# Performance work log

Hardware: AMD Instinct MI355X
Metric: run time of the kernel (lower is better)

Reference implementation:

```python
import jax, jax.numpy as jnp
import numpy as np

B, T, DA, DZ, K = 2048, 256, 20, 4, 3


def setup_inputs() -> dict:
    key = jax.random.key(0)
    k1, k2, k3, k4 = jax.random.split(key, 4)
    a = jax.random.normal(k1, (B, T, DA), dtype=jnp.float32)
    alpha_logits = jax.random.normal(k2, (B, T, K), dtype=jnp.float32)
    # original inits: A = eye per mixture component, C = 0.05*randn
    A_base = jnp.tile(jnp.eye(DZ, dtype=jnp.float32), (K, 1, 1)) \
             + 0.01 * jax.random.normal(k3, (K, DZ, DZ), dtype=jnp.float32)
    C_base = 0.05 * jax.random.normal(k4, (K, DA, DZ), dtype=jnp.float32)
    return {"a": a, "alpha_logits": alpha_logits, "A_base": A_base, "C_base": C_base}


def _kvae_smooth(a, alpha_logits, A_base, C_base):
    alpha = jax.nn.softmax(alpha_logits, axis=-1)          # [B,T,K]
    Q = 0.08 * jnp.eye(DZ, dtype=a.dtype)
    R = 0.03 * jnp.eye(DA, dtype=a.dtype)
    std_min = 1e-4 * jnp.eye(DZ, dtype=a.dtype)
    I_z = jnp.eye(DZ, dtype=a.dtype)
    z0 = jnp.zeros((B, DZ), dtype=a.dtype)
    std0 = 20.0 * jnp.broadcast_to(I_z, (B, DZ, DZ))

    def filt_step(carry, xs):
        z_prev, std_prev = carry                            # [B,dz], [B,dz,dz]
        a_t, alpha_t = xs                                   # [B,da], [B,K]
        Ai = jnp.einsum('bk,kij->bij', alpha_t, A_base)     # [B,dz,dz]
        Ci = jnp.einsum('bk,kij->bij', alpha_t, C_base)     # [B,da,dz]
        # --- prediction ---
        z_hat = jnp.einsum('bij,bj->bi', Ai, z_prev)
        std_hat = Ai @ std_prev @ Ai.transpose(0, 2, 1) + Q
        std_hat_c = jnp.maximum(std_hat, std_min)           # stored (clipped) version
        # --- update (uses unclipped std_hat, as in the original) ---
        resid = a_t - jnp.einsum('bij,bj->bi', Ci, z_hat)
        S = Ci @ std_hat @ Ci.transpose(0, 2, 1) + R        # [B,da,da]
        Kg = std_hat @ Ci.transpose(0, 2, 1) @ jnp.linalg.inv(S)
        post_z = z_hat + jnp.einsum('bij,bj->bi', Kg, resid)
        IKC = I_z - Kg @ Ci
        post_std = IKC @ std_hat @ IKC.transpose(0, 2, 1) + Kg @ R @ Kg.transpose(0, 2, 1)
        return (post_z, post_std), (z_hat, std_hat_c, post_z, post_std, Ai)

    _, (z_hat_a, std_hat_a, post_z_a, post_std_a, A_a) = jax.lax.scan(
        filt_step, (z0, std0), (a.transpose(1, 0, 2), alpha.transpose(1, 0, 2)))
    # stacked arrays are time-major: [T, B, ...]

    last_z, last_std = post_z_a[-1], post_std_a[-1]

    def smooth_step(carry, xs):
        pz_s, ps_s = carry
        post_z_jm1, post_std_jm1, A_j, std_hat_j, z_hat_j = xs
        D = post_std_jm1 @ A_j.transpose(0, 2, 1) @ jnp.linalg.inv(std_hat_j)
        z_s = post_z_jm1 + jnp.einsum('bij,bj->bi', D, pz_s - z_hat_j)
        s_s = post_std_jm1 + D @ (ps_s - std_hat_j) @ D.transpose(0, 2, 1)
        return (z_s, s_s), (z_s, s_s)

    xs = (post_z_a[:-1], post_std_a[:-1], A_a[1:], std_hat_a[1:], z_hat_a[1:])
    _, (z_sm, s_sm) = jax.lax.scan(smooth_step, (last_z, last_std), xs, reverse=True)
    # z_sm: [T-1, B, dz] in forward time order; append last filtered state
    z_smooth = jnp.concatenate([z_sm, last_z[None]], axis=0).transpose(1, 0, 2)          # [B,T,dz]
    std_smooth = jnp.concatenate([s_sm, last_std[None]], axis=0).transpose(1, 0, 2, 3)   # [B,T,dz,dz]
    return z_smooth, std_smooth


def reference(a, alpha_logits, A_base, C_base):
    return _kvae_smooth(a, alpha_logits, A_base, C_base)
```

## Files before the change

### kernel.cpp

```cpp
#include <hip/hip_runtime.h>

#define BB 2048
#define TT 256
#define DA 20
#define DZ 4
#define KK 3
#define NC 64
#define CL 4
#define NCH (BB*NC)
#define QQ 0.08f
#define RINV (1.0f/0.03f)

__device__ __forceinline__ void sym_expand(const float* s, float* f){
  f[0]=s[0];  f[1]=s[1];  f[2]=s[2];  f[3]=s[3];
  f[4]=s[1];  f[5]=s[4];  f[6]=s[5];  f[7]=s[6];
  f[8]=s[2];  f[9]=s[5];  f[10]=s[7]; f[11]=s[8];
  f[12]=s[3]; f[13]=s[6]; f[14]=s[8]; f[15]=s[9];
}
__device__ __forceinline__ void sym_from_full(const float* F, float* s){
  s[0]=F[0]; s[1]=0.5f*(F[1]+F[4]); s[2]=0.5f*(F[2]+F[8]); s[3]=0.5f*(F[3]+F[12]);
  s[4]=F[5]; s[5]=0.5f*(F[6]+F[9]); s[6]=0.5f*(F[7]+F[13]);
  s[7]=F[10]; s[8]=0.5f*(F[11]+F[14]); s[9]=F[15];
}

__device__ __forceinline__ void inv4(const float* m, float* b){
  float s0 = m[0]*m[5]  - m[4]*m[1];
  float s1 = m[0]*m[6]  - m[4]*m[2];
  float s2 = m[0]*m[7]  - m[4]*m[3];
  float s3 = m[1]*m[6]  - m[5]*m[2];
  float s4 = m[1]*m[7]  - m[5]*m[3];
  float s5 = m[2]*m[7]  - m[6]*m[3];
  float c5 = m[10]*m[15] - m[14]*m[11];
  float c4 = m[9]*m[15]  - m[13]*m[11];
  float c3 = m[9]*m[14]  - m[13]*m[10];
  float c2 = m[8]*m[15]  - m[12]*m[11];
  float c1 = m[8]*m[14]  - m[12]*m[10];
  float c0 = m[8]*m[13]  - m[12]*m[9];
  float det = s0*c5 - s1*c4 + s2*c3 + s3*c2 - s4*c1 + s5*c0;
  float id = 1.0f/det;
  b[0]  = ( m[5]*c5  - m[6]*c4  + m[7]*c3 )*id;
  b[1]  = (-m[1]*c5  + m[2]*c4  - m[3]*c3 )*id;
  b[2]  = ( m[13]*s5 - m[14]*s4 + m[15]*s3)*id;
  b[3]  = (-m[9]*s5  + m[10]*s4 - m[11]*s3)*id;
  b[4]  = (-m[4]*c5  + m[6]*c2  - m[7]*c1 )*id;
  b[5]  = ( m[0]*c5  - m[2]*c2  + m[3]*c1 )*id;
  b[6]  = (-m[12]*s5 + m[14]*s2 - m[15]*s1)*id;
  b[7]  = ( m[8]*s5  - m[10]*s2 + m[11]*s1)*id;
  b[8]  = ( m[4]*c4  - m[5]*c2  + m[7]*c0 )*id;
  b[9]  = (-m[0]*c4  + m[1]*c2  - m[3]*c0 )*id;
  b[10] = ( m[12]*s4 - m[13]*s2 + m[15]*s0)*id;
  b[11] = (-m[8]*s4  + m[9]*s2  - m[11]*s0)*id;
  b[12] = (-m[4]*c3  + m[5]*c1  - m[6]*c0 )*id;
  b[13] = ( m[0]*c3  - m[1]*c1  + m[2]*c0 )*id;
  b[14] = (-m[12]*s3 + m[13]*s1 - m[14]*s0)*id;
  b[15] = ( m[8]*s3  - m[9]*s1  + m[10]*s0)*id;
}

__device__ __forceinline__ void mm4(const float* A, const float* Bm, float* C){
  #pragma unroll
  for (int i=0;i<4;i++){
    #pragma unroll
    for (int j=0;j<4;j++){
      float acc = A[i*4+0]*Bm[0*4+j];
      acc = fmaf(A[i*4+1], Bm[1*4+j], acc);
      acc = fmaf(A[i*4+2], Bm[2*4+j], acc);
      acc = fmaf(A[i*4+3], Bm[3*4+j], acc);
      C[i*4+j] = acc;
    }
  }
}
__device__ __forceinline__ void mm4_bt(const float* A, const float* Bm, float* C){
  #pragma unroll
  for (int i=0;i<4;i++){
    #pragma unroll
    for (int j=0;j<4;j++){
      float acc = A[i*4+0]*Bm[j*4+0];
      acc = fmaf(A[i*4+1], Bm[j*4+1], acc);
      acc = fmaf(A[i*4+2], Bm[j*4+2], acc);
      acc = fmaf(A[i*4+3], Bm[j*4+3], acc);
      C[i*4+j] = acc;
    }
  }
}
__device__ __forceinline__ void mm4_at(const float* A, const float* Bm, float* C){
  #pragma unroll
  for (int i=0;i<4;i++){
    #pragma unroll
    for (int j=0;j<4;j++){
      float acc = A[0*4+i]*Bm[0*4+j];
      acc = fmaf(A[1*4+i], Bm[1*4+j], acc);
      acc = fmaf(A[2*4+i], Bm[2*4+j], acc);
      acc = fmaf(A[3*4+i], Bm[3*4+j], acc);
      C[i*4+j] = acc;
    }
  }
}
__device__ __forceinline__ void mv4(const float* M, const float* v, float* o){
  #pragma unroll
  for (int i=0;i<4;i++)
    o[i] = fmaf(M[i*4+3],v[3],fmaf(M[i*4+2],v[2],fmaf(M[i*4+1],v[1],M[i*4+0]*v[0])));
}
__device__ __forceinline__ void mv4_t(const float* M, const float* v, float* o){
  #pragma unroll
  for (int i=0;i<4;i++)
    o[i] = fmaf(M[12+i],v[3],fmaf(M[8+i],v[2],fmaf(M[4+i],v[1],M[i]*v[0])));
}

__device__ __forceinline__ void mix_from_regs(
    const float4* avq, float l0, float l1, float l2,
    const float* sA, const float* sC,
    float* Am, float* G, float* w)
{
  float mx = fmaxf(l0, fmaxf(l1,l2));
  float e0=expf(l0-mx), e1=expf(l1-mx), e2=expf(l2-mx);
  float is = 1.0f/(e0+e1+e2);
  float a0=e0*is, a1=e1*is, a2=e2*is;
  #pragma unroll
  for (int c=0;c<16;c++) Am[c] = fmaf(a0,sA[c],fmaf(a1,sA[16+c],a2*sA[32+c]));
  float av[20]={avq[0].x,avq[0].y,avq[0].z,avq[0].w, avq[1].x,avq[1].y,avq[1].z,avq[1].w,
                avq[2].x,avq[2].y,avq[2].z,avq[2].w, avq[3].x,avq[3].y,avq[3].z,avq[3].w,
                avq[4].x,avq[4].y,avq[4].z,avq[4].w};
  #pragma unroll
  for (int c=0;c<10;c++) G[c]=0.f;
  w[0]=0.f;w[1]=0.f;w[2]=0.f;w[3]=0.f;
  #pragma unroll
  for (int d=0; d<DA; d++){
    float ad = av[d];
    float c0 = fmaf(a0, sC[d*4+0], fmaf(a1, sC[80+d*4+0], a2*sC[160+d*4+0]));
    float c1 = fmaf(a0, sC[d*4+1], fmaf(a1, sC[80+d*4+1], a2*sC[160+d*4+1]));
    float c2 = fmaf(a0, sC[d*4+2], fmaf(a1, sC[80+d*4+2], a2*sC[160+d*4+2]));
    float c3 = fmaf(a0, sC[d*4+3], fmaf(a1, sC[80+d*4+3], a2*sC[160+d*4+3]));
    w[0]=fmaf(c0,ad,w[0]); w[1]=fmaf(c1,ad,w[1]); w[2]=fmaf(c2,ad,w[2]); w[3]=fmaf(c3,ad,w[3]);
    G[0]=fmaf(c0,c0,G[0]); G[1]=fmaf(c0,c1,G[1]); G[2]=fmaf(c0,c2,G[2]); G[3]=fmaf(c0,c3,G[3]);
    G[4]=fmaf(c1,c1,G[4]); G[5]=fmaf(c1,c2,G[5]); G[6]=fmaf(c1,c3,G[6]);
    G[7]=fmaf(c2,c2,G[7]); G[8]=fmaf(c2,c3,G[8]);
    G[9]=fmaf(c3,c3,G[9]);
  }
  #pragma unroll
  for (int c=0;c<10;c++) G[c]*=RINV;
  #pragma unroll
  for (int c=0;c<4;c++)  w[c]*=RINV;
}

__device__ __forceinline__ void elem_build(const float* Am, const float* G, const float* w,
    float* Ae, float* be, float* Ce, float* he, float* Je)
{
  float Gf[16]; sym_expand(G,Gf);
  float N[16];
  #pragma unroll
  for (int i=0;i<16;i++) N[i] = QQ*Gf[i];
  N[0]+=1.f; N[5]+=1.f; N[10]+=1.f; N[15]+=1.f;
  float Phi[16]; inv4(N,Phi);
  mm4(Phi, Am, Ae);
  float Pw[4]; mv4(Phi, w, Pw);
  #pragma unroll
  for (int i=0;i<4;i++) be[i]=QQ*Pw[i];
  mv4_t(Am, Pw, he);
  float PhiG[16]; mm4(Phi, Gf, PhiG);
  float U[16]; mm4_at(Am, PhiG, U);
  float Jf[16]; mm4(U, Am, Jf);
  sym_from_full(Jf, Je);
  float Cf[16];
  #pragma unroll
  for (int i=0;i<16;i++) Cf[i]=QQ*Phi[i];
  sym_from_full(Cf, Ce);
}

__device__ __forceinline__ void compose(float* Ar, float* br, float* Cr, float* hr, float* Jr,
    const float* Ae, const float* be, const float* Ce, const float* he, const float* Je)
{
  float Crf[16]; sym_expand(Cr,Crf);
  float Jef[16]; sym_expand(Je,Jef);
  float N[16]; mm4(Crf,Jef,N);
  N[0]+=1.f; N[5]+=1.f; N[10]+=1.f; N[15]+=1.f;
  float E[16]; inv4(N,E);
  float EA[16]; mm4(E,Ar,EA);
  float Anew[16]; mm4(Ae,EA,Anew);
  float t1[4]; mv4(Crf,he,t1);
  #pragma unroll
  for (int i=0;i<4;i++) t1[i]+=br[i];
  float t2[4]; mv4(E,t1,t2);
  float bnew[4]; mv4(Ae,t2,bnew);
  #pragma unroll
  for (int i=0;i<4;i++) bnew[i]+=be[i];
  float EC[16]; mm4(E,Crf,EC);
  float AEC[16]; mm4(Ae,EC,AEC);
  float Cfull[16]; mm4_bt(AEC,Ae,Cfull);
  float Cnew[10]; sym_from_full(Cfull,Cnew);
  #pragma unroll
  for (int i=0;i<10;i++) Cnew[i]+=Ce[i];
  float v[4]; mv4(Jef,br,v);
  #pragma unroll
  for (int i=0;i<4;i++) v[i]=he[i]-v[i];
  float Ev[4]; mv4_t(E,v,Ev);
  float hnew[4]; mv4_t(Ar,Ev,hnew);
  #pragma unroll
  for (int i=0;i<4;i++) hnew[i]+=hr[i];
  float EtJ[16]; mm4_at(E,Jef,EtJ);
  float AtEtJ[16]; mm4_at(Ar,EtJ,AtEtJ);
  float Jfull[16]; mm4(AtEtJ,Ar,Jfull);
  float Jnew[10]; sym_from_full(Jfull,Jnew);
  #pragma unroll
  for (int i=0;i<10;i++) Jnew[i]+=Jr[i];
  #pragma unroll
  for (int i=0;i<16;i++) Ar[i]=Anew[i];
  #pragma unroll
  for (int i=0;i<4;i++){ br[i]=bnew[i]; hr[i]=hnew[i]; }
  #pragma unroll
  for (int i=0;i<10;i++){ Cr[i]=Cnew[i]; Jr[i]=Jnew[i]; }
}

__device__ __forceinline__ void elem_apply(const float* Ae, const float* be, const float* Ce,
    const float* he, const float* Je, float* m, float* S)
{
  float Pf[16]; sym_expand(S,Pf);
  float Jf[16]; sym_expand(Je,Jf);
  float N[16]; mm4(Pf,Jf,N);
  N[0]+=1.f; N[5]+=1.f; N[10]+=1.f; N[15]+=1.f;
  float T[16]; inv4(N,T);
  float t1[4]; mv4(Pf,he,t1);
  #pragma unroll
  for (int i=0;i<4;i++) t1[i]+=m[i];
  float t2[4]; mv4(T,t1,t2);
  float mn[4]; mv4(Ae,t2,mn);
  #pragma unroll
  for (int i=0;i<4;i++) mn[i]+=be[i];
  float TP[16]; mm4(T,Pf,TP);
  float ATP[16]; mm4(Ae,TP,ATP);
  float Pn[16]; mm4_bt(ATP,Ae,Pn);
  float Sn[10]; sym_from_full(Pn,Sn);
  #pragma unroll
  for (int i=0;i<10;i++) S[i]=Sn[i]+Ce[i];
  #pragma unroll
  for (int i=0;i<4;i++) m[i]=mn[i];
}

__device__ __forceinline__ void sm_build(const float* A1, const float* Pc1,
    const float* Mj, const float* pzj, float* D, float* e, float* F)
{
  float Pcf[16]; sym_expand(Pc1,Pcf);
  float E[16]; inv4(Pcf,E);
  float Mf[16]; sym_expand(Mj,Mf);
  float MB[16]; mm4_bt(Mf,A1,MB);
  mm4(MB,E,D);
  float zh[4]; mv4(A1,pzj,zh);
  float Dzh[4]; mv4(D,zh,Dzh);
  #pragma unroll
  for (int i=0;i<4;i++) e[i]=pzj[i]-Dzh[i];
  float U[16]; mm4(D,Pcf,U);
  float W[16]; mm4_bt(U,D,W);
  float Ws[10]; sym_from_full(W,Ws);
  #pragma unroll
  for (int i=0;i<10;i++) F[i]=Mj[i]-Ws[i];
}

__device__ __forceinline__ void sm_apply(const float* D, const float* e, const float* F,
    float* z, float* S)
{
  float zn[4]; mv4(D,z,zn);
  #pragma unroll
  for (int i=0;i<4;i++) z[i]=zn[i]+e[i];
  float Sf[16]; sym_expand(S,Sf);
  float U[16]; mm4(D,Sf,U);
  float W[16]; mm4_bt(U,D,W);
  float Sn[10]; sym_from_full(W,Sn);
  #pragma unroll
  for (int i=0;i<10;i++) S[i]=Sn[i]+F[i];
}

__device__ __forceinline__ void aff_pre(float* Dr, float* er, float* Fr,
    const float* Dk, const float* ek, const float* Fk)
{
  float Dn[16]; mm4(Dk,Dr,Dn);
  float t1[4]; mv4(Dk,er,t1);
  float Frf[16]; sym_expand(Fr,Frf);
  float U[16]; mm4(Dk,Frf,U);
  float W[16]; mm4_bt(U,Dk,W);
  float Ws[10]; sym_from_full(W,Ws);
  #pragma unroll
  for (int i=0;i<4;i++) er[i]=t1[i]+ek[i];
  #pragma unroll
  for (int i=0;i<10;i++) Fr[i]=Ws[i]+Fk[i];
  #pragma unroll
  for (int i=0;i<16;i++) Dr[i]=Dn[i];
}

__global__ __launch_bounds__(256) void k_fwd(
    const float* __restrict__ a, const float* __restrict__ logits,
    const float* __restrict__ Abase, const float* __restrict__ Cbase,
    float4* __restrict__ fbound)
{
  __shared__ float sA[KK*16];
  __shared__ float sC[KK*DA*DZ];
  for (int i=threadIdx.x;i<KK*16;i+=256) sA[i]=Abase[i];
  for (int i=threadIdx.x;i<KK*DA*DZ;i+=256) sC[i]=Cbase[i];
  __syncthreads();
  int lane = threadIdx.x & 63;
  int b = blockIdx.x*4 + (threadIdx.x>>6);
  int c = lane;

  const float4* lgp = (const float4*)(logits + ((size_t)b*TT + c*CL)*KK);
  float4 lq0=lgp[0], lq1=lgp[1], lq2=lgp[2];
  float lgf[12]={lq0.x,lq0.y,lq0.z,lq0.w, lq1.x,lq1.y,lq1.z,lq1.w, lq2.x,lq2.y,lq2.z,lq2.w};
  const float4* ap = (const float4*)(a + ((size_t)b*TT + c*CL)*DA);

  float X[44];
  #pragma unroll 1
  for (int s=0;s<CL;s++){
    float4 av[5];
    #pragma unroll
    for (int i=0;i<5;i++) av[i]=ap[s*5+i];
    float Am[16], G[10], w[4];
    mix_from_regs(av, lgf[s*3+0], lgf[s*3+1], lgf[s*3+2], sA, sC, Am, G, w);
    float Ae[16], be[4], Ce[10], he[4], Je[10];
    elem_build(Am,G,w,Ae,be,Ce,he,Je);
    if (s==0){
      #pragma unroll
      for (int i=0;i<16;i++) X[i]=Ae[i];
      #pragma unroll
      for (int i=0;i<4;i++){ X[16+i]=be[i]; X[30+i]=he[i]; }
      #pragma unroll
      for (int i=0;i<10;i++){ X[20+i]=Ce[i]; X[34+i]=Je[i]; }
    } else {
      compose(X, X+16, X+20, X+30, X+34, Ae, be, Ce, he, Je);
    }
  }

  #pragma unroll 1
  for (int d=1; d<NC; d<<=1){
    float P[44];
    #pragma unroll
    for (int i=0;i<44;i++) P[i] = __shfl_up(X[i], d, 64);
    if (lane >= d){
      compose(P, P+16, P+20, P+30, P+34, X, X+16, X+20, X+30, X+34);
      #pragma unroll
      for (int i=0;i<44;i++) X[i]=P[i];
    }
  }

  float Pm[44];
  #pragma unroll
  for (int i=0;i<44;i++) Pm[i] = __shfl_up(X[i], 1, 64);
  float m[4]={0.f,0.f,0.f,0.f};
  float S[10]={20.f,0.f,0.f,0.f,20.f,0.f,0.f,20.f,0.f,20.f};
  if (lane > 0) elem_apply(Pm, Pm+16, Pm+20, Pm+30, Pm+34, m, S);

  float4 ob[4]; float* po=(float*)ob;
  #pragma unroll
  for (int i=0;i<4;i++) po[i]=m[i];
  #pragma unroll
  for (int i=0;i<10;i++) po[4+i]=S[i];
  po[14]=0.f; po[15]=0.f;
  float4* dst = fbound + ((size_t)b*NC + c)*4;
  #pragma unroll
  for (int p=0;p<4;p++) dst[p]=ob[p];
}

__global__ __launch_bounds__(256) void k_freplay(
    const float* __restrict__ a, const float* __restrict__ logits,
    const float* __restrict__ Abase, const float* __restrict__ Cbase,
    const float4* __restrict__ fbound,
    float4* __restrict__ el, float4* __restrict__ bF0, float4* __restrict__ bL7)
{
  __shared__ float sA[KK*16];
  __shared__ float sC[KK*DA*DZ];
  for (int i=threadIdx.x;i<KK*16;i+=256) sA[i]=Abase[i];
  for (int i=threadIdx.x;i<KK*DA*DZ;i+=256) sC[i]=Cbase[i];
  __syncthreads();
  int tid = blockIdx.x*256+threadIdx.x;
  int b = tid & (BB-1);
  int c = tid >> 11;
  float4 fb[4];
  const float4* fsrc = fbound + ((size_t)b*NC + c)*4;
  #pragma unroll
  for (int p=0;p<4;p++) fb[p]=fsrc[p];
  const float* pf=(const float*)fb;
  float z[4]={pf[0],pf[1],pf[2],pf[3]};
  float S[10]={pf[4],pf[5],pf[6],pf[7],pf[8],pf[9],pf[10],pf[11],pf[12],pf[13]};
  const float4* lgp = (const float4*)(logits + ((size_t)b*TT + c*CL)*KK);
  float4 lq0=lgp[0], lq1=lgp[1], lq2=lgp[2];
  float lgf[12]={lq0.x,lq0.y,lq0.z,lq0.w, lq1.x,lq1.y,lq1.z,lq1.w, lq2.x,lq2.y,lq2.z,lq2.w};
  const float4* ap = (const float4*)(a + ((size_t)b*TT + c*CL)*DA);
  float4 av[5], avn[5];
  #pragma unroll
  for (int i=0;i<5;i++) av[i]=ap[i];

  float Mprev[10], pzprev[4];
  #pragma unroll 1
  for (int s=0;s<CL;s++){
    if (s+1<CL){
      #pragma unroll
      for (int i=0;i<5;i++) avn[i]=ap[(s+1)*5+i];
    }
    float Am[16], G[10], w[4];
    mix_from_regs(av, lgf[s*3+0], lgf[s*3+1], lgf[s*3+2], sA, sC, Am, G, w);
    float zh[4];
    mv4(Am,z,zh);
    float Sf[16]; sym_expand(S,Sf);
    float AS[16]; mm4(Am,Sf,AS);
    float P[10];
    {
      int cc=0;
      #pragma unroll
      for (int i=0;i<4;i++){
        #pragma unroll
        for (int j=0;j<4;j++){
          if (j<i) continue;
          float acc = AS[i*4+0]*Am[j*4+0];
          acc = fmaf(AS[i*4+1],Am[j*4+1],acc);
          acc = fmaf(AS[i*4+2],Am[j*4+2],acc);
          acc = fmaf(AS[i*4+3],Am[j*4+3],acc);
          if (i==j) acc += QQ;
          P[cc++] = acc;
        }
      }
    }
    float Pf[16]; sym_expand(P,Pf);
    float Gf[16]; sym_expand(G,Gf);
    float N[16]; mm4(Pf,Gf,N);
    N[0]+=1.f; N[5]+=1.f; N[10]+=1.f; N[15]+=1.f;
    float Ninv[16]; inv4(N,Ninv);
    float Mf[16]; mm4(Ninv,Pf,Mf);
    float M[10]; sym_from_full(Mf,M);
    float u[4];
    #pragma unroll
    for (int i=0;i<4;i++)
      u[i] = w[i] - fmaf(Gf[i*4+3],zh[3],fmaf(Gf[i*4+2],zh[2],fmaf(Gf[i*4+1],zh[1],Gf[i*4+0]*zh[0])));
    float Ms[16]; sym_expand(M,Ms);
    float pz[4];
    #pragma unroll
    for (int i=0;i<4;i++)
      pz[i] = zh[i] + fmaf(Ms[i*4+3],u[3],fmaf(Ms[i*4+2],u[2],fmaf(Ms[i*4+1],u[1],Ms[i*4+0]*u[0])));
    float Pc[10];
    Pc[0]=fmaxf(P[0],1e-4f); Pc[1]=fmaxf(P[1],0.f); Pc[2]=fmaxf(P[2],0.f); Pc[3]=fmaxf(P[3],0.f);
    Pc[4]=fmaxf(P[4],1e-4f); Pc[5]=fmaxf(P[5],0.f); Pc[6]=fmaxf(P[6],0.f);
    Pc[7]=fmaxf(P[7],1e-4f); Pc[8]=fmaxf(P[8],0.f);
    Pc[9]=fmaxf(P[9],1e-4f);

    if (s==0){
      float4 f0[7]; float* p0=(float*)f0;
      #pragma unroll
      for (int i=0;i<16;i++) p0[i]=Am[i];
      #pragma unroll
      for (int i=0;i<10;i++) p0[16+i]=Pc[i];
      p0[26]=0.f; p0[27]=0.f;
      float4* d0 = bF0 + ((size_t)b*NC + c)*7;
      #pragma unroll
      for (int p=0;p<7;p++) d0[p]=f0[p];
    } else {
      float D[16], e[4], F[10];
      sm_build(Am, Pc, Mprev, pzprev, D, e, F);
      float4 eb[8]; float* pe2=(float*)eb;
      #pragma unroll
      for (int i=0;i<16;i++) pe2[i]=D[i];
      #pragma unroll
      for (int i=0;i<4;i++) pe2[16+i]=e[i];
      #pragma unroll
      for (int i=0;i<10;i++) pe2[20+i]=F[i];
      pe2[30]=0.f; pe2[31]=0.f;
      float4* de = el + (((size_t)b*NC + c)*CL + (s-1))*8;
      #pragma unroll
      for (int p=0;p<8;p++) de[p]=eb[p];
    }
    #pragma unroll
    for (int i=0;i<10;i++) Mprev[i]=M[i];
    #pragma unroll
    for (int i=0;i<4;i++) pzprev[i]=pz[i];
    #pragma unroll
    for (int i=0;i<4;i++) z[i]=pz[i];
    #pragma unroll
    for (int i=0;i<10;i++) S[i]=M[i];
    #pragma unroll
    for (int i=0;i<5;i++) av[i]=avn[i];
  }
  float4 l7[4]; float* pl=(float*)l7;
  #pragma unroll
  for (int i=0;i<10;i++) pl[i]=Mprev[i];
  #pragma unroll
  for (int i=0;i<4;i++) pl[10+i]=pzprev[i];
  pl[14]=0.f; pl[15]=0.f;
  float4* dl = bL7 + ((size_t)b*NC + c)*4;
  #pragma unroll
  for (int p=0;p<4;p++) dl[p]=l7[p];
}

__global__ __launch_bounds__(256) void k_bwd(
    float4* __restrict__ el, const float4* __restrict__ bF0, const float4* __restrict__ bL7,
    float4* __restrict__ sbound)
{
  int lane = threadIdx.x & 63;
  int b = blockIdx.x*4 + (threadIdx.x>>6);
  int c = lane;

  float Y[30];
  int kstart;
  if (c < NC-1){
    float4 l7[4];
    const float4* sl = bL7 + ((size_t)b*NC + c)*4;
    #pragma unroll
    for (int p=0;p<4;p++) l7[p]=sl[p];
    float4 f0[7];
    const float4* s0 = bF0 + ((size_t)b*NC + (c+1))*7;
    #pragma unroll
    for (int p=0;p<7;p++) f0[p]=s0[p];
    const float* pl=(const float*)l7;
    const float* p0=(const float*)f0;
    float M7[10]={pl[0],pl[1],pl[2],pl[3],pl[4],pl[5],pl[6],pl[7],pl[8],pl[9]};
    float pz7[4]={pl[10],pl[11],pl[12],pl[13]};
    float A0[16];
    #pragma unroll
    for (int i=0;i<16;i++) A0[i]=p0[i];
    float Pc0[10];
    #pragma unroll
    for (int i=0;i<10;i++) Pc0[i]=p0[16+i];
    sm_build(A0,Pc0,M7,pz7, Y, Y+16, Y+20);
    float4 eb[8]; float* pe2=(float*)eb;
    #pragma unroll
    for (int i=0;i<16;i++) pe2[i]=Y[i];
    #pragma unroll
    for (int i=0;i<4;i++) pe2[16+i]=Y[16+i];
    #pragma unroll
    for (int i=0;i<10;i++) pe2[20+i]=Y[20+i];
    pe2[30]=0.f; pe2[31]=0.f;
    float4* de = el + (((size_t)b*NC + c)*CL + (CL-1))*8;
    #pragma unroll
    for (int p=0;p<8;p++) de[p]=eb[p];
    kstart = CL-2;
  } else {
    float4 eb[8];
    const float4* se = el + (((size_t)b*NC + c)*CL + (CL-2))*8;
    #pragma unroll
    for (int p=0;p<8;p++) eb[p]=se[p];
    const float* pe=(const float*)eb;
    #pragma unroll
    for (int i=0;i<30;i++) Y[i]=pe[i];
    kstart = CL-3;
  }
  #pragma unroll 1
  for (int k=kstart;k>=0;k--){
    float4 eb[8];
    const float4* se = el + (((size_t)b*NC + c)*CL + k)*8;
    #pragma unroll
    for (int p=0;p<8;p++) eb[p]=se[p];
    const float* pe=(const float*)eb;
    aff_pre(Y, Y+16, Y+20, pe, pe+16, pe+20);
  }

  #pragma unroll 1
  for (int d=1; d<NC; d<<=1){
    float P[30];
    #pragma unroll
    for (int i=0;i<30;i++) P[i] = __shfl_down(Y[i], d, 64);
    if (c + d < NC){
      aff_pre(P, P+16, P+20, Y, Y+16, Y+20);
      #pragma unroll
      for (int i=0;i<30;i++) Y[i]=P[i];
    }
  }

  const float4* tl = bL7 + ((size_t)b*NC + (NC-1))*4;
  float4 t0=tl[0],t1q=tl[1],t2q=tl[2],t3q=tl[3];
  const float* pt=(const float*)&t0;
  float S[10]={t0.x,t0.y,t0.z,t0.w, t1q.x,t1q.y,t1q.z,t1q.w, t2q.x,t2q.y};
  float z[4]={t2q.z,t2q.w,t3q.x,t3q.y};
  (void)pt;

  float Pn[30];
  #pragma unroll
  for (int i=0;i<30;i++) Pn[i] = __shfl_down(Y[i], 1, 64);
  if (c < NC-1) sm_apply(Pn, Pn+16, Pn+20, z, S);

  float4 ob[4]; float* po=(float*)ob;
  #pragma unroll
  for (int i=0;i<4;i++) po[i]=z[i];
  #pragma unroll
  for (int i=0;i<10;i++) po[4+i]=S[i];
  po[14]=0.f; po[15]=0.f;
  float4* dst = sbound + ((size_t)b*NC + c)*4;
  #pragma unroll
  for (int p=0;p<4;p++) dst[p]=ob[p];
}

__global__ __launch_bounds__(256) void k_sreplay(
    const float4* __restrict__ el, const float4* __restrict__ sbound,
    float* __restrict__ out)
{
  int tid = blockIdx.x*256+threadIdx.x;
  int b = tid & (BB-1);
  int c = tid >> 11;
  const size_t Z0 = (size_t)BB*TT*DZ;
  float4 sb[4];
  const float4* ssrc = sbound + ((size_t)b*NC + c)*4;
  #pragma unroll
  for (int p=0;p<4;p++) sb[p]=ssrc[p];
  const float* ps=(const float*)sb;
  float z[4]={ps[0],ps[1],ps[2],ps[3]};
  float S[10]={ps[4],ps[5],ps[6],ps[7],ps[8],ps[9],ps[10],ps[11],ps[12],ps[13]};
  int ktop = (c==NC-1) ? (CL-2) : (CL-1);
  float4 cur[8], nxt[8];
  const float4* base = el + ((size_t)b*NC + c)*CL*8;
  #pragma unroll
  for (int p=0;p<8;p++) cur[p]=base[ktop*8+p];
  if (c==NC-1){
    *(float4*)(out + ((size_t)b*TT + (TT-1))*DZ) = make_float4(z[0],z[1],z[2],z[3]);
    float Sf[16]; sym_expand(S,Sf);
    float4* so=(float4*)(out + Z0 + ((size_t)b*TT + (TT-1))*16);
    so[0]=make_float4(Sf[0],Sf[1],Sf[2],Sf[3]);
    so[1]=make_float4(Sf[4],Sf[5],Sf[6],Sf[7]);
    so[2]=make_float4(Sf[8],Sf[9],Sf[10],Sf[11]);
    so[3]=make_float4(Sf[12],Sf[13],Sf[14],Sf[15]);
  }
  #pragma unroll 1
  for (int k=ktop;k>=0;k--){
    if (k-1 >= 0){
      #pragma unroll
      for (int p=0;p<8;p++) nxt[p]=base[(k-1)*8+p];
    }
    const float* pe=(const float*)cur;
    sm_apply(pe, pe+16, pe+20, z, S);
    int j = c*CL + k;
    *(float4*)(out + ((size_t)b*TT + j)*DZ) = make_float4(z[0],z[1],z[2],z[3]);
    float Sf[16]; sym_expand(S,Sf);
    float4* so=(float4*)(out + Z0 + ((size_t)b*TT + j)*16);
    so[0]=make_float4(Sf[0],Sf[1],Sf[2],Sf[3]);
    so[1]=make_float4(Sf[4],Sf[5],Sf[6],Sf[7]);
    so[2]=make_float4(Sf[8],Sf[9],Sf[10],Sf[11]);
    so[3]=make_float4(Sf[12],Sf[13],Sf[14],Sf[15]);
    #pragma unroll
    for (int p=0;p<8;p++) cur[p]=nxt[p];
  }
}

extern "C" void kernel_launch(void* const* d_in, const int* in_sizes, int n_in,
                              void* d_out, int out_size, void* d_ws, size_t ws_size,
                              hipStream_t stream) {
  const float* a      = (const float*)d_in[0];
  const float* logits = (const float*)d_in[1];
  const float* Abase  = (const float*)d_in[2];
  const float* Cbase  = (const float*)d_in[3];
  float* out = (float*)d_out;

  float4* ws4 = (float4*)d_ws;
  float4* fbound = ws4;
  float4* el     = fbound + (size_t)4*NCH;
  float4* bF0    = el     + (size_t)32*NCH;
  float4* bL7    = bF0    + (size_t)7*NCH;
  float4* sbound = bL7    + (size_t)4*NCH;

  k_fwd    <<<dim3(BB/4),   dim3(256), 0, stream>>>(a, logits, Abase, Cbase, fbound);
  k_freplay<<<dim3(NCH/256),dim3(256), 0, stream>>>(a, logits, Abase, Cbase, fbound, el, bF0, bL7);
  k_bwd    <<<dim3(BB/4),   dim3(256), 0, stream>>>(el, bF0, bL7, sbound);
  k_sreplay<<<dim3(NCH/256),dim3(256), 0, stream>>>(el, sbound, out);
}
```

Measured before the change: 253.6 us.

## Fuse forward replay into scan kernel and smoothing replay into backward scan

The forward chunk scan kernel now replays its own chunk right after the prefix composition. The cross-chunk boundary element is built from the neighbour's first-step data exchanged through shared memory, so the fbound, bF0 and bL7 workspace round trips and one launch go away. The backward scan kernel likewise replays the smoothed outputs directly instead of writing sbound and launching k_sreplay. This cuts four launches to two and removes global traffic, but the replay now runs with the scan kernels' batch-major thread mapping, where each wave handles the 64 chunks of one batch. That may change memory coalescing for the el and output accesses and raises register and shared-memory pressure.

```diff
diff --git a/kernel.cpp b/kernel.cpp
--- a/kernel.cpp
+++ b/kernel.cpp
@@ -288,10 +288,11 @@
 __global__ __launch_bounds__(256) void k_fwd(
     const float* __restrict__ a, const float* __restrict__ logits,
     const float* __restrict__ Abase, const float* __restrict__ Cbase,
-    float4* __restrict__ fbound)
+    float4* __restrict__ el, float4* __restrict__ term)
 {
   __shared__ float sA[KK*16];
   __shared__ float sC[KK*DA*DZ];
+  __shared__ float stash[256*26];
   for (int i=threadIdx.x;i<KK*16;i+=256) sA[i]=Abase[i];
   for (int i=threadIdx.x;i<KK*DA*DZ;i+=256) sC[i]=Cbase[i];
   __syncthreads();
@@ -337,61 +338,19 @@
       for (int i=0;i<44;i++) X[i]=P[i];
     }
   }
-
   float Pm[44];
   #pragma unroll
   for (int i=0;i<44;i++) Pm[i] = __shfl_up(X[i], 1, 64);
-  float m[4]={0.f,0.f,0.f,0.f};
+  float z[4]={0.f,0.f,0.f,0.f};
   float S[10]={20.f,0.f,0.f,0.f,20.f,0.f,0.f,20.f,0.f,20.f};
-  if (lane > 0) elem_apply(Pm, Pm+16, Pm+20, Pm+30, Pm+34, m, S);
-
-  float4 ob[4]; float* po=(float*)ob;
-  #pragma unroll
-  for (int i=0;i<4;i++) po[i]=m[i];
-  #pragma unroll
-  for (int i=0;i<10;i++) po[4+i]=S[i];
-  po[14]=0.f; po[15]=0.f;
-  float4* dst = fbound + ((size_t)b*NC + c)*4;
-  #pragma unroll
-  for (int p=0;p<4;p++) dst[p]=ob[p];
-}
-
-__global__ __launch_bounds__(256) void k_freplay(
-    const float* __restrict__ a, const float* __restrict__ logits,
-    const float* __restrict__ Abase, const float* __restrict__ Cbase,
-    const float4* __restrict__ fbound,
-    float4* __restrict__ el, float4* __restrict__ bF0, float4* __restrict__ bL7)
-{
-  __shared__ float sA[KK*16];
-  __shared__ float sC[KK*DA*DZ];
-  for (int i=threadIdx.x;i<KK*16;i+=256) sA[i]=Abase[i];
-  for (int i=threadIdx.x;i<KK*DA*DZ;i+=256) sC[i]=Cbase[i];
-  __syncthreads();
-  int tid = blockIdx.x*256+threadIdx.x;
-  int b = tid & (BB-1);
-  int c = tid >> 11;
-  float4 fb[4];
-  const float4* fsrc = fbound + ((size_t)b*NC + c)*4;
-  #pragma unroll
-  for (int p=0;p<4;p++) fb[p]=fsrc[p];
-  const float* pf=(const float*)fb;
-  float z[4]={pf[0],pf[1],pf[2],pf[3]};
-  float S[10]={pf[4],pf[5],pf[6],pf[7],pf[8],pf[9],pf[10],pf[11],pf[12],pf[13]};
-  const float4* lgp = (const float4*)(logits + ((size_t)b*TT + c*CL)*KK);
-  float4 lq0=lgp[0], lq1=lgp[1], lq2=lgp[2];
-  float lgf[12]={lq0.x,lq0.y,lq0.z,lq0.w, lq1.x,lq1.y,lq1.z,lq1.w, lq2.x,lq2.y,lq2.z,lq2.w};
-  const float4* ap = (const float4*)(a + ((size_t)b*TT + c*CL)*DA);
-  float4 av[5], avn[5];
-  #pragma unroll
-  for (int i=0;i<5;i++) av[i]=ap[i];
-
-  float Mprev[10], pzprev[4];
+  if (lane > 0) elem_apply(Pm, Pm+16, Pm+20, Pm+30, Pm+34, z, S);
+
+  float* myst = stash + threadIdx.x*26;
   #pragma unroll 1
   for (int s=0;s<CL;s++){
-    if (s+1<CL){
-      #pragma unroll
-      for (int i=0;i<5;i++) avn[i]=ap[(s+1)*5+i];
-    }
+    float4 av[5];
+    #pragma unroll
+    for (int i=0;i<5;i++) av[i]=ap[s*5+i];
     float Am[16], G[10], w[4];
     mix_from_regs(av, lgf[s*3+0], lgf[s*3+1], lgf[s*3+2], sA, sC, Am, G, w);
     float zh[4];
@@ -415,6 +374,33 @@
         }
       }
     }
+    float Pc[10];
+    Pc[0]=fmaxf(P[0],1e-4f); Pc[1]=fmaxf(P[1],0.f); Pc[2]=fmaxf(P[2],0.f); Pc[3]=fmaxf(P[3],0.f);
+    Pc[4]=fmaxf(P[4],1e-4f); Pc[5]=fmaxf(P[5],0.f); Pc[6]=fmaxf(P[6],0.f);
+    Pc[7]=fmaxf(P[7],1e-4f); Pc[8]=fmaxf(P[8],0.f);
+    Pc[9]=fmaxf(P[9],1e-4f);
+
+    if (s==0){
+      #pragma unroll
+      for (int i=0;i<16;i++) myst[i]=Am[i];
+      #pragma unroll
+      for (int i=0;i<10;i++) myst[16+i]=Pc[i];
+    } else {
+      float D[16], e[4], F[10];
+      sm_build(Am, Pc, S, z, D, e, F);
+      float4 eb[8]; float* pe2=(float*)eb;
+      #pragma unroll
+      for (int i=0;i<16;i++) pe2[i]=D[i];
+      #pragma unroll
+      for (int i=0;i<4;i++) pe2[16+i]=e[i];
+      #pragma unroll
+      for (int i=0;i<10;i++) pe2[20+i]=F[i];
+      pe2[30]=0.f; pe2[31]=0.f;
+      float4* de = el + (((size_t)b*NC + c)*CL + (s-1))*8;
+      #pragma unroll
+      for (int p=0;p<8;p++) de[p]=eb[p];
+    }
+
     float Pf[16]; sym_expand(P,Pf);
     float Gf[16]; sym_expand(G,Gf);
     float N[16]; mm4(Pf,Gf,N);
@@ -427,121 +413,73 @@
     for (int i=0;i<4;i++)
       u[i] = w[i] - fmaf(Gf[i*4+3],zh[3],fmaf(Gf[i*4+2],zh[2],fmaf(Gf[i*4+1],zh[1],Gf[i*4+0]*zh[0])));
     float Ms[16]; sym_expand(M,Ms);
-    float pz[4];
     #pragma unroll
     for (int i=0;i<4;i++)
-      pz[i] = zh[i] + fmaf(Ms[i*4+3],u[3],fmaf(Ms[i*4+2],u[2],fmaf(Ms[i*4+1],u[1],Ms[i*4+0]*u[0])));
-    float Pc[10];
-    Pc[0]=fmaxf(P[0],1e-4f); Pc[1]=fmaxf(P[1],0.f); Pc[2]=fmaxf(P[2],0.f); Pc[3]=fmaxf(P[3],0.f);
-    Pc[4]=fmaxf(P[4],1e-4f); Pc[5]=fmaxf(P[5],0.f); Pc[6]=fmaxf(P[6],0.f);
-    Pc[7]=fmaxf(P[7],1e-4f); Pc[8]=fmaxf(P[8],0.f);
-    Pc[9]=fmaxf(P[9],1e-4f);
-
-    if (s==0){
-      float4 f0[7]; float* p0=(float*)f0;
-      #pragma unroll
-      for (int i=0;i<16;i++) p0[i]=Am[i];
-      #pragma unroll
-      for (int i=0;i<10;i++) p0[16+i]=Pc[i];
-      p0[26]=0.f; p0[27]=0.f;
-      float4* d0 = bF0 + ((size_t)b*NC + c)*7;
-      #pragma unroll
-      for (int p=0;p<7;p++) d0[p]=f0[p];
-    } else {
-      float D[16], e[4], F[10];
-      sm_build(Am, Pc, Mprev, pzprev, D, e, F);
-      float4 eb[8]; float* pe2=(float*)eb;
-      #pragma unroll
-      for (int i=0;i<16;i++) pe2[i]=D[i];
-      #pragma unroll
-      for (int i=0;i<4;i++) pe2[16+i]=e[i];
-      #pragma unroll
-      for (int i=0;i<10;i++) pe2[20+i]=F[i];
-      pe2[30]=0.f; pe2[31]=0.f;
-      float4* de = el + (((size_t)b*NC + c)*CL + (s-1))*8;
-      #pragma unroll
-      for (int p=0;p<8;p++) de[p]=eb[p];
-    }
-    #pragma unroll
-    for (int i=0;i<10;i++) Mprev[i]=M[i];
-    #pragma unroll
-    for (int i=0;i<4;i++) pzprev[i]=pz[i];
-    #pragma unroll
-    for (int i=0;i<4;i++) z[i]=pz[i];
+      z[i] = zh[i] + fmaf(Ms[i*4+3],u[3],fmaf(Ms[i*4+2],u[2],fmaf(Ms[i*4+1],u[1],Ms[i*4+0]*u[0])));
     #pragma unroll
     for (int i=0;i<10;i++) S[i]=M[i];
-    #pragma unroll
-    for (int i=0;i<5;i++) av[i]=avn[i];
-  }
-  float4 l7[4]; float* pl=(float*)l7;
-  #pragma unroll
-  for (int i=0;i<10;i++) pl[i]=Mprev[i];
-  #pragma unroll
-  for (int i=0;i<4;i++) pl[10+i]=pzprev[i];
-  pl[14]=0.f; pl[15]=0.f;
-  float4* dl = bL7 + ((size_t)b*NC + c)*4;
-  #pragma unroll
-  for (int p=0;p<4;p++) dl[p]=l7[p];
+  }
+  __syncthreads();
+
+  if (c < NC-1){
+    const float* nst = stash + (threadIdx.x+1)*26;
+    float A0[16], Pc0[10];
+    #pragma unroll
+    for (int i=0;i<16;i++) A0[i]=nst[i];
+    #pragma unroll
+    for (int i=0;i<10;i++) Pc0[i]=nst[16+i];
+    float D[16], e[4], F[10];
+    sm_build(A0, Pc0, S, z, D, e, F);
+    float4 eb[8]; float* pe2=(float*)eb;
+    #pragma unroll
+    for (int i=0;i<16;i++) pe2[i]=D[i];
+    #pragma unroll
+    for (int i=0;i<4;i++) pe2[16+i]=e[i];
+    #pragma unroll
+    for (int i=0;i<10;i++) pe2[20+i]=F[i];
+    pe2[30]=0.f; pe2[31]=0.f;
+    float4* de = el + (((size_t)b*NC + c)*CL + (CL-1))*8;
+    #pragma unroll
+    for (int p=0;p<8;p++) de[p]=eb[p];
+  } else {
+    float4 tb[4]; float* pt=(float*)tb;
+    #pragma unroll
+    for (int i=0;i<10;i++) pt[i]=S[i];
+    #pragma unroll
+    for (int i=0;i<4;i++) pt[10+i]=z[i];
+    pt[14]=0.f; pt[15]=0.f;
+    float4* dt = term + (size_t)b*4;
+    #pragma unroll
+    for (int p=0;p<4;p++) dt[p]=tb[p];
+  }
 }
 
 __global__ __launch_bounds__(256) void k_bwd(
-    float4* __restrict__ el, const float4* __restrict__ bF0, const float4* __restrict__ bL7,
-    float4* __restrict__ sbound)
+    const float4* __restrict__ el, const float4* __restrict__ term,
+    float* __restrict__ out)
 {
   int lane = threadIdx.x & 63;
   int b = blockIdx.x*4 + (threadIdx.x>>6);
   int c = lane;
+  const float4* base = el + ((size_t)b*NC + c)*CL*8;
 
   float Y[30];
   int kstart;
-  if (c < NC-1){
-    float4 l7[4];
-    const float4* sl = bL7 + ((size_t)b*NC + c)*4;
-    #pragma unroll
-    for (int p=0;p<4;p++) l7[p]=sl[p];
-    float4 f0[7];
-    const float4* s0 = bF0 + ((size_t)b*NC + (c+1))*7;
-    #pragma unroll
-    for (int p=0;p<7;p++) f0[p]=s0[p];
-    const float* pl=(const float*)l7;
-    const float* p0=(const float*)f0;
-    float M7[10]={pl[0],pl[1],pl[2],pl[3],pl[4],pl[5],pl[6],pl[7],pl[8],pl[9]};
-    float pz7[4]={pl[10],pl[11],pl[12],pl[13]};
-    float A0[16];
-    #pragma unroll
-    for (int i=0;i<16;i++) A0[i]=p0[i];
-    float Pc0[10];
-    #pragma unroll
-    for (int i=0;i<10;i++) Pc0[i]=p0[16+i];
-    sm_build(A0,Pc0,M7,pz7, Y, Y+16, Y+20);
-    float4 eb[8]; float* pe2=(float*)eb;
-    #pragma unroll
-    for (int i=0;i<16;i++) pe2[i]=Y[i];
-    #pragma unroll
-    for (int i=0;i<4;i++) pe2[16+i]=Y[16+i];
-    #pragma unroll
-    for (int i=0;i<10;i++) pe2[20+i]=Y[20+i];
-    pe2[30]=0.f; pe2[31]=0.f;
-    float4* de = el + (((size_t)b*NC + c)*CL + (CL-1))*8;
-    #pragma unroll
-    for (int p=0;p<8;p++) de[p]=eb[p];
-    kstart = CL-2;
-  } else {
+  {
+    int k0 = (c < NC-1) ? (CL-1) : (CL-2);
     float4 eb[8];
-    const float4* se = el + (((size_t)b*NC + c)*CL + (CL-2))*8;
-    #pragma unroll
-    for (int p=0;p<8;p++) eb[p]=se[p];
+    #pragma unroll
+    for (int p=0;p<8;p++) eb[p]=base[k0*8+p];
     const float* pe=(const float*)eb;
     #pragma unroll
     for (int i=0;i<30;i++) Y[i]=pe[i];
-    kstart = CL-3;
+    kstart = k0-1;
   }
   #pragma unroll 1
   for (int k=kstart;k>=0;k--){
     float4 eb[8];
-    const float4* se = el + (((size_t)b*NC + c)*CL + k)*8;
-    #pragma unroll
-    for (int p=0;p<8;p++) eb[p]=se[p];
+    #pragma unroll
+    for (int p=0;p<8;p++) eb[p]=base[k*8+p];
     const float* pe=(const float*)eb;
     aff_pre(Y, Y+16, Y+20, pe, pe+16, pe+20);
   }
@@ -558,47 +496,20 @@
     }
   }
 
-  const float4* tl = bL7 + ((size_t)b*NC + (NC-1))*4;
-  float4 t0=tl[0],t1q=tl[1],t2q=tl[2],t3q=tl[3];
-  const float* pt=(const float*)&t0;
+  const float4* tp = term + (size_t)b*4;
+  float4 t0=tp[0], t1q=tp[1], t2q=tp[2], t3q=tp[3];
   float S[10]={t0.x,t0.y,t0.z,t0.w, t1q.x,t1q.y,t1q.z,t1q.w, t2q.x,t2q.y};
   float z[4]={t2q.z,t2q.w,t3q.x,t3q.y};
-  (void)pt;
+  (void)t3q;
 
   float Pn[30];
   #pragma unroll
   for (int i=0;i<30;i++) Pn[i] = __shfl_down(Y[i], 1, 64);
   if (c < NC-1) sm_apply(Pn, Pn+16, Pn+20, z, S);
 
-  float4 ob[4]; float* po=(float*)ob;
-  #pragma unroll
-  for (int i=0;i<4;i++) po[i]=z[i];
-  #pragma unroll
-  for (int i=0;i<10;i++) po[4+i]=S[i];
-  po[14]=0.f; po[15]=0.f;
-  float4* dst = sbound + ((size_t)b*NC + c)*4;
-  #pragma unroll
-  for (int p=0;p<4;p++) dst[p]=ob[p];
-}
-
-__global__ __launch_bounds__(256) void k_sreplay(
-    const float4* __restrict__ el, const float4* __restrict__ sbound,
-    float* __restrict__ out)
-{
-  int tid = blockIdx.x*256+threadIdx.x;
-  int b = tid & (BB-1);
-  int c = tid >> 11;
   const size_t Z0 = (size_t)BB*TT*DZ;
-  float4 sb[4];
-  const float4* ssrc = sbound + ((size_t)b*NC + c)*4;
-  #pragma unroll
-  for (int p=0;p<4;p++) sb[p]=ssrc[p];
-  const float* ps=(const float*)sb;
-  float z[4]={ps[0],ps[1],ps[2],ps[3]};
-  float S[10]={ps[4],ps[5],ps[6],ps[7],ps[8],ps[9],ps[10],ps[11],ps[12],ps[13]};
   int ktop = (c==NC-1) ? (CL-2) : (CL-1);
   float4 cur[8], nxt[8];
-  const float4* base = el + ((size_t)b*NC + c)*CL*8;
   #pragma unroll
   for (int p=0;p<8;p++) cur[p]=base[ktop*8+p];
   if (c==NC-1){
@@ -641,14 +552,9 @@
   float* out = (float*)d_out;
 
   float4* ws4 = (float4*)d_ws;
-  float4* fbound = ws4;
-  float4* el     = fbound + (size_t)4*NCH;
-  float4* bF0    = el     + (size_t)32*NCH;
-  float4* bL7    = bF0    + (size_t)7*NCH;
-  float4* sbound = bL7    + (size_t)4*NCH;
-
-  k_fwd    <<<dim3(BB/4),   dim3(256), 0, stream>>>(a, logits, Abase, Cbase, fbound);
-  k_freplay<<<dim3(NCH/256),dim3(256), 0, stream>>>(a, logits, Abase, Cbase, fbound, el, bF0, bL7);
-  k_bwd    <<<dim3(BB/4),   dim3(256), 0, stream>>>(el, bF0, bL7, sbound);
-  k_sreplay<<<dim3(NCH/256),dim3(256), 0, stream>>>(el, sbound, out);
-}
+  float4* el   = ws4;
+  float4* term = el + (size_t)CL*8*NCH;
+
+  k_fwd<<<dim3(BB/4), dim3(256), 0, stream>>>(a, logits, Abase, Cbase, el, term);
+  k_bwd<<<dim3(BB/4), dim3(256), 0, stream>>>(el, term, out);
+}
```

Result: faster. 215.8 us (-14.9%).
